# Optimization experiments

Hardware: AMD Instinct MI355X
Metric: run time of the kernel (lower is better)

Reference implementation:

```python
import jax, jax.numpy as jnp
import numpy as np

T, B, IN, H, L, C = 512, 4096, 12, 32, 10, 4


def setup_inputs() -> dict:
    key = jax.random.key(0)
    ks = jax.random.split(key, 12)
    s = 1.0 / np.sqrt(H)  # PyTorch GRU init scale ~ U(-1/sqrt(H), 1/sqrt(H))
    return {
        "x": jax.random.normal(ks[0], (T, B, IN), jnp.float32),
        "W_ih0": jax.random.normal(ks[1], (3 * H, IN), jnp.float32) * s,
        "W_hh0": jax.random.normal(ks[2], (3 * H, H), jnp.float32) * s,
        "b_ih0": jax.random.normal(ks[3], (3 * H,), jnp.float32) * s,
        "b_hh0": jax.random.normal(ks[4], (3 * H,), jnp.float32) * s,
        "W_ih": jax.random.normal(ks[5], (L - 1, 3 * H, H), jnp.float32) * s,
        "W_hh": jax.random.normal(ks[6], (L - 1, 3 * H, H), jnp.float32) * s,
        "b_ih": jax.random.normal(ks[7], (L - 1, 3 * H), jnp.float32) * s,
        "b_hh": jax.random.normal(ks[8], (L - 1, 3 * H), jnp.float32) * s,
        "fc_W": jax.random.normal(ks[9], (C, H), jnp.float32) * s,
        "fc_b": jax.random.normal(ks[10], (C,), jnp.float32) * s,
        "lengths": jax.random.randint(ks[11], (B,), 1, T + 1, jnp.int32),
    }


def gru_cell(x_t, h, Wi, Wh, bi, bh):
    # PyTorch GRU cell math
    gi = x_t @ Wi.T + bi          # [B, 3H]
    gh = h @ Wh.T + bh            # [B, 3H]
    i_r, i_z, i_n = jnp.split(gi, 3, axis=-1)
    h_r, h_z, h_n = jnp.split(gh, 3, axis=-1)
    r = jax.nn.sigmoid(i_r + h_r)
    z = jax.nn.sigmoid(i_z + h_z)
    n = jnp.tanh(i_n + r * h_n)
    return (1.0 - z) * n + z * h


def reference(x, W_ih0, W_hh0, b_ih0, b_hh0, W_ih, W_hh, b_ih, b_hh, fc_W, fc_b, lengths):
    Bn = x.shape[1]
    h0 = jnp.zeros((L, Bn, H), x.dtype)

    def step(h, x_t):
        hs = []
        inp = x_t
        for l in range(L):
            if l == 0:
                hl = gru_cell(inp, h[0], W_ih0, W_hh0, b_ih0, b_hh0)
            else:
                hl = gru_cell(inp, h[l], W_ih[l - 1], W_hh[l - 1], b_ih[l - 1], b_hh[l - 1])
            hs.append(hl)
            inp = hl
        return jnp.stack(hs), inp  # carry all-layer hidden, emit top-layer output

    _, outs = jax.lax.scan(step, h0, x)  # [T, B, H]
    idx = jnp.maximum(lengths, 1) - 1    # last valid timestep per sequence
    last = outs[idx, jnp.arange(Bn)]     # [B, H]
    logits = last @ fc_W.T + fc_b        # [B, C]
    return jax.nn.log_softmax(logits, axis=1)
```

## Files before the change

### kernel.cpp

```cpp
#include <hip/hip_runtime.h>
#include <math.h>

#define TT 512
#define BB 4096
#define IN_DIM 12
#define HH 32
#define LL 10
#define CC 4
#define NTH (LL * 64)

typedef _Float16 half8 __attribute__((ext_vector_type(8)));
typedef _Float16 half4 __attribute__((ext_vector_type(4)));
typedef float f32x4 __attribute__((ext_vector_type(4)));

#define LOG2E 1.44269504088896340736f

#define H_HI 0
#define H_LO (LL * 4 * 512)
#define X_HI (H_LO + LL * 2 * 512)
#define LDS16_TOT (X_HI + 2 * 512)

#define MFMA_(A, B, C) C = __builtin_amdgcn_mfma_f32_16x16x32_f16(A, B, C, 0, 0, 0)

__global__ __launch_bounds__(NTH, 2)
void gru_fused_mfma(const float* __restrict__ x,
                    const float* __restrict__ Wih0,
                    const float* __restrict__ Whh0,
                    const float* __restrict__ bih0,
                    const float* __restrict__ bhh0,
                    const float* __restrict__ Wih,
                    const float* __restrict__ Whh,
                    const float* __restrict__ bih,
                    const float* __restrict__ bhh,
                    const int*   __restrict__ lengths,
                    float*       __restrict__ last)
{
    __shared__ __align__(16) _Float16 lds16[LDS16_TOT];
    __shared__ int flagS[LL];
    __shared__ int rflagS[LL];

    const int tid  = threadIdx.x;
    const int w    = tid >> 6;
    const int lane = tid & 63;
    const int bi16 = lane & 15;
    const int quad = lane >> 4;
    const int bg   = blockIdx.x;

    {
        float4 z4 = make_float4(0.f, 0.f, 0.f, 0.f);
        float4* p = (float4*)lds16;
        for (int i = tid; i < LDS16_TOT / 8; i += NTH) p[i] = z4;
    }
    if (lane == 0) { flagS[w] = -1; rflagS[w] = -1; }
    __syncthreads();

    const float *Wi, *Wh, *bivec, *bhvec;
    int wistride;
    if (w == 0) { Wi = Wih0; Wh = Whh0; bivec = bih0; bhvec = bhh0; wistride = IN_DIM; }
    else {
        Wi = Wih + (size_t)(w - 1) * 96 * HH;
        Wh = Whh + (size_t)(w - 1) * 96 * HH;
        bivec = bih + (size_t)(w - 1) * 96;
        bhvec = bhh + (size_t)(w - 1) * 96;
        wistride = HH;
    }

    const int frow[12] = {0, 0, 16, 16, 32, 32, 48, 48, 64, 80, 64, 80};
    const int fchk[12] = {0, 1, 0, 1, 0, 1, 0, 1, 0, 0, 1, 1};
    half8 Whi[12], Wlo[6];
#pragma unroll
    for (int f = 0; f < 12; f++) {
        const float sc = (f < 8) ? -LOG2E : 2.0f * LOG2E;
        int row = frow[f] + bi16;
        const float* src; int kin;
        if (fchk[f] == 0) { src = Wi + (size_t)row * wistride; kin = wistride; }
        else              { src = Wh + (size_t)row * HH;       kin = HH; }
        int wloidx = (f < 8) ? (f >> 1) : (f - 6);
#pragma unroll
        for (int kk = 0; kk < 8; kk++) {
            int k = quad * 8 + kk;
            float v = (k < kin) ? src[k] * sc : 0.0f;
            _Float16 h = (_Float16)v;
            Whi[f][kk] = h;
            if (fchk[f] == 1) Wlo[wloidx][kk] = (_Float16)(v - (float)h);
        }
    }

    f32x4 biasreg[8];
#pragma unroll
    for (int ct = 0; ct < 8; ct++) {
        int g = ct >> 1, jt = ct & 1;
#pragma unroll
        for (int r = 0; r < 4; r++) {
            int j = jt * 16 + quad * 4 + r;
            float v;
            if      (g == 0) v = -(bivec[j]      + bhvec[j])      * LOG2E;
            else if (g == 1) v = -(bivec[32 + j] + bhvec[32 + j]) * LOG2E;
            else if (g == 2) v = bivec[64 + j] * (2.0f * LOG2E);
            else             v = bhvec[64 + j] * (2.0f * LOG2E);
            biasreg[ct][r] = v;
        }
    }

    int capT = -1;
    if (w == LL - 1) {
        int len = lengths[bg * 16 + bi16];
        capT = ((len < 1) ? 1 : len) - 1;
    }

    const int laneoff = lane * 8;
    const int inbase  = (w == 0) ? X_HI : (H_HI + (w - 1) * 2048);
    const int inmask  = (w == 0) ? 1 : 3;
    const int ownhi   = H_HI + w * 2048;
    const int ownlo   = H_LO + w * 1024;
    const int wibase  = (quad >> 1) * 128 + bi16 * 8 + (quad & 1) * 4;

    const int xbb = lane / 3, xkg = lane - xbb * 3;
    const int xq   = (xkg == 2) ? 1 : 0;
    const int xoff = (xkg == 1) ? 4 : 0;
    const int xidx = xq * 128 + xbb * 8 + xoff;
    const bool xlane = (w == 0) && (lane < 48);

    auto stage_x = [&](const float4& xl, int t) {
        half4 h4;
        h4[0] = (_Float16)xl.x; h4[1] = (_Float16)xl.y;
        h4[2] = (_Float16)xl.z; h4[3] = (_Float16)xl.w;
        *(half4*)(lds16 + X_HI + ((t & 1) << 9) + xidx) = h4;
    };

    if (xlane) {
        float4 x0 = *(const float4*)(x + (size_t)bg * 192 + lane * 4);
        float4 x1 = *(const float4*)(x + (size_t)BB * IN_DIM + (size_t)bg * 192 + lane * 4);
        stage_x(x0, 0);
        stage_x(x1, 1);
    }

    float hprev[8] = {0, 0, 0, 0, 0, 0, 0, 0};
    __syncthreads();

    auto substep = [&](int t) {
        half8 bxh = *(const half8*)(lds16 + inbase + ((t & inmask) << 9) + laneoff);
        half8 bhh = *(const half8*)(lds16 + ownhi + (((t + 3) & 3) << 9) + laneoff);
        half8 bhl = *(const half8*)(lds16 + ownlo + (((t + 1) & 1) << 9) + laneoff);

        f32x4 acc[8];

#pragma unroll
        for (int ct = 0; ct < 4; ct++) {
            acc[ct] = __builtin_amdgcn_mfma_f32_16x16x32_f16(
                          Whi[ct * 2 + 0], bxh, biasreg[ct], 0, 0, 0);
            MFMA_(Whi[ct * 2 + 1], bhh, acc[ct]);
            MFMA_(Whi[ct * 2 + 1], bhl, acc[ct]);
            MFMA_(Wlo[ct],         bhh, acc[ct]);
        }
#pragma unroll
        for (int jt = 0; jt < 2; jt++) {
            acc[4 + jt] = __builtin_amdgcn_mfma_f32_16x16x32_f16(
                              Whi[8 + jt], bxh, biasreg[4 + jt], 0, 0, 0);
            acc[6 + jt] = __builtin_amdgcn_mfma_f32_16x16x32_f16(
                              Whi[10 + jt], bhh, biasreg[6 + jt], 0, 0, 0);
            MFMA_(Whi[10 + jt], bhl, acc[6 + jt]);
            MFMA_(Wlo[4 + jt],  bhh, acc[6 + jt]);
        }

#pragma unroll
        for (int jt = 0; jt < 2; jt++) {
            f32x4 R = acc[0 + jt], Z = acc[2 + jt];
            f32x4 IN_ = acc[4 + jt], HN = acc[6 + jt];
            half4 h4, l4;
            float hv[4];
#pragma unroll
            for (int pr = 0; pr < 2; pr++) {
                const int r0 = pr * 2, r1 = pr * 2 + 1;
                float a0 = 1.0f + __builtin_amdgcn_exp2f(R[r0]);
                float b0 = 1.0f + __builtin_amdgcn_exp2f(Z[r0]);
                float a1 = 1.0f + __builtin_amdgcn_exp2f(R[r1]);
                float b1 = 1.0f + __builtin_amdgcn_exp2f(Z[r1]);
                float p0 = a0 * b0, p1 = a1 * b1;
                float q  = __builtin_amdgcn_rcpf(p0 * p1);
                float q0 = q * p1, q1 = q * p0;
                float rv0 = q0 * b0, zv0 = q0 * a0;
                float rv1 = q1 * b1, zv1 = q1 * a1;
                float ea0 = __builtin_amdgcn_exp2f(fmaf(rv0, HN[r0], IN_[r0]));
                float ea1 = __builtin_amdgcn_exp2f(fmaf(rv1, HN[r1], IN_[r1]));
                float d0 = ea0 + 1.0f, d1 = ea1 + 1.0f;
                float qn = __builtin_amdgcn_rcpf(d0 * d1);
                float nv0 = fmaf(-2.0f, qn * d1, 1.0f);
                float nv1 = fmaf(-2.0f, qn * d0, 1.0f);
                float h0 = fmaf(zv0, hprev[jt * 4 + r0] - nv0, nv0);
                float h1 = fmaf(zv1, hprev[jt * 4 + r1] - nv1, nv1);
                hprev[jt * 4 + r0] = h0;
                hprev[jt * 4 + r1] = h1;
                _Float16 hh0 = (_Float16)h0, hh1 = (_Float16)h1;
                h4[r0] = hh0; h4[r1] = hh1;
                l4[r0] = (_Float16)(h0 - (float)hh0);
                l4[r1] = (_Float16)(h1 - (float)hh1);
                hv[r0] = h0; hv[r1] = h1;
            }
            int wi = jt * 256 + wibase;
            *(half4*)(lds16 + ownhi + ((t & 3) << 9) + wi) = h4;
            *(half4*)(lds16 + ownlo + ((t & 1) << 9) + wi) = l4;
            if (w == LL - 1 && t == capT) {
                float4 o = make_float4(hv[0], hv[1], hv[2], hv[3]);
                *(float4*)(last + (size_t)(bg * 16 + bi16) * HH + jt * 16 + quad * 4) = o;
            }
        }
    };

    for (int t = 0; t < TT; t += 2) {
        if (w > 0) {
            while (__hip_atomic_load(&flagS[w - 1], __ATOMIC_ACQUIRE,
                                     __HIP_MEMORY_SCOPE_WORKGROUP) < t + 1)
                __builtin_amdgcn_s_sleep(1);
        }
        if (w < LL - 1) {
            while (__hip_atomic_load(&rflagS[w], __ATOMIC_ACQUIRE,
                                     __HIP_MEMORY_SCOPE_WORKGROUP) < t - 3)
                __builtin_amdgcn_s_sleep(1);
        }

        float4 xa0, xa1;
        bool dl0 = false, dl1 = false;
        if (xlane) {
            if (t + 2 < TT) {
                xa0 = *(const float4*)(x + (size_t)(t + 2) * BB * IN_DIM +
                                       (size_t)bg * 192 + lane * 4);
                dl0 = true;
            }
            if (t + 3 < TT) {
                xa1 = *(const float4*)(x + (size_t)(t + 3) * BB * IN_DIM +
                                       (size_t)bg * 192 + lane * 4);
                dl1 = true;
            }
        }

        substep(t);
        substep(t + 1);

        if (dl0) stage_x(xa0, t + 2);
        if (dl1) stage_x(xa1, t + 3);

        if (lane == 0) {
            if (w < LL - 1)
                __hip_atomic_store(&flagS[w], t + 1, __ATOMIC_RELEASE,
                                   __HIP_MEMORY_SCOPE_WORKGROUP);
            if (w > 0)
                __hip_atomic_store(&rflagS[w - 1], t + 1, __ATOMIC_RELEASE,
                                   __HIP_MEMORY_SCOPE_WORKGROUP);
        }
    }
}

__global__ __launch_bounds__(256)
void fc_head(const float* __restrict__ last,
             const float* __restrict__ fcW,
             const float* __restrict__ fcb,
             float* __restrict__ out)
{
    int b = blockIdx.x * blockDim.x + threadIdx.x;
    if (b >= BB) return;
    float lg[CC];
#pragma unroll
    for (int c = 0; c < CC; c++) lg[c] = fcb[c];
#pragma unroll
    for (int j = 0; j < HH; j++) {
        float h = last[(size_t)b * HH + j];
#pragma unroll
        for (int c = 0; c < CC; c++) lg[c] = fmaf(fcW[c * HH + j], h, lg[c]);
    }
    float m = lg[0];
#pragma unroll
    for (int c = 1; c < CC; c++) m = fmaxf(m, lg[c]);
    float s = 0.0f;
#pragma unroll
    for (int c = 0; c < CC; c++) s += __expf(lg[c] - m);
    float lse = m + logf(s);
#pragma unroll
    for (int c = 0; c < CC; c++) out[(size_t)b * CC + c] = lg[c] - lse;
}

extern "C" void kernel_launch(void* const* d_in, const int* in_sizes, int n_in,
                              void* d_out, int out_size, void* d_ws, size_t ws_size,
                              hipStream_t stream)
{
    const float* x    = (const float*)d_in[0];
    const float* Wih0 = (const float*)d_in[1];
    const float* Whh0 = (const float*)d_in[2];
    const float* bih0 = (const float*)d_in[3];
    const float* bhh0 = (const float*)d_in[4];
    const float* Wih  = (const float*)d_in[5];
    const float* Whh  = (const float*)d_in[6];
    const float* bih  = (const float*)d_in[7];
    const float* bhh  = (const float*)d_in[8];
    const float* fcW  = (const float*)d_in[9];
    const float* fcb  = (const float*)d_in[10];
    const int*   lens = (const int*)d_in[11];
    float* out = (float*)d_out;

    float* last = (float*)d_ws;

    gru_fused_mfma<<<dim3(BB / 16), dim3(NTH), 0, stream>>>(
        x, Wih0, Whh0, bih0, bhh0, Wih, Whh, bih, bhh, lens, last);

    fc_head<<<dim3(BB / 256), dim3(256), 0, stream>>>(last, fcW, fcb, out);
}
```

Before: 955.6 us.

## Pack ten GRU layers onto four waves with skewed wavefront schedule

Each workgroup now has 4 waves instead of 10, and each wave owns 2 or 3 layers. The layers run in a diagonal (skewed) schedule so that dependent cells within a round read hidden states written in earlier rounds, and inter-wave flags sync once per round. The low-half weight corrections move from registers to LDS so three layers' high-half weights fit in registers. This cuts the wave count and flag traffic and lets one wave interleave independent layer cells. The cost is more serial work per wave and extra LDS reads on every cell.

```diff
diff --git a/kernel.cpp b/kernel.cpp
--- a/kernel.cpp
+++ b/kernel.cpp
@@ -7,7 +7,7 @@
 #define HH 32
 #define LL 10
 #define CC 4
-#define NTH (LL * 64)
+#define NTH 256
 
 typedef _Float16 half8 __attribute__((ext_vector_type(8)));
 typedef _Float16 half4 __attribute__((ext_vector_type(4)));
@@ -19,10 +19,13 @@
 #define H_LO (LL * 4 * 512)
 #define X_HI (H_LO + LL * 2 * 512)
 #define LDS16_TOT (X_HI + 2 * 512)
+#define WLO_TOT (LL * 6 * 512)
 
 #define MFMA_(A, B, C) C = __builtin_amdgcn_mfma_f32_16x16x32_f16(A, B, C, 0, 0, 0)
 
-__global__ __launch_bounds__(NTH, 2)
+template<int N> struct IC { static constexpr int value = N; };
+
+__global__ __launch_bounds__(NTH, 1)
 void gru_fused_mfma(const float* __restrict__ x,
                     const float* __restrict__ Wih0,
                     const float* __restrict__ Whh0,
@@ -36,8 +39,9 @@
                     float*       __restrict__ last)
 {
     __shared__ __align__(16) _Float16 lds16[LDS16_TOT];
-    __shared__ int flagS[LL];
-    __shared__ int rflagS[LL];
+    __shared__ __align__(16) _Float16 wlo16[WLO_TOT];
+    __shared__ int flagE[3];
+    __shared__ int rflagE[3];
 
     const int tid  = threadIdx.x;
     const int w    = tid >> 6;
@@ -46,74 +50,92 @@
     const int quad = lane >> 4;
     const int bg   = blockIdx.x;
 
+    const int myStart = (w == 0) ? 0 : (w == 1) ? 2 : (w == 2) ? 5 : 8;
+    const int myCnt   = (w == 0 || w == 3) ? 2 : 3;
+
     {
         float4 z4 = make_float4(0.f, 0.f, 0.f, 0.f);
         float4* p = (float4*)lds16;
         for (int i = tid; i < LDS16_TOT / 8; i += NTH) p[i] = z4;
     }
-    if (lane == 0) { flagS[w] = -1; rflagS[w] = -1; }
-    __syncthreads();
-
-    const float *Wi, *Wh, *bivec, *bhvec;
-    int wistride;
-    if (w == 0) { Wi = Wih0; Wh = Whh0; bivec = bih0; bhvec = bhh0; wistride = IN_DIM; }
-    else {
-        Wi = Wih + (size_t)(w - 1) * 96 * HH;
-        Wh = Whh + (size_t)(w - 1) * 96 * HH;
-        bivec = bih + (size_t)(w - 1) * 96;
-        bhvec = bhh + (size_t)(w - 1) * 96;
-        wistride = HH;
-    }
+    if (tid < 3) { flagE[tid] = -1; rflagE[tid] = -1; }
 
     const int frow[12] = {0, 0, 16, 16, 32, 32, 48, 48, 64, 80, 64, 80};
     const int fchk[12] = {0, 1, 0, 1, 0, 1, 0, 1, 0, 0, 1, 1};
-    half8 Whi[12], Wlo[6];
-#pragma unroll
-    for (int f = 0; f < 12; f++) {
-        const float sc = (f < 8) ? -LOG2E : 2.0f * LOG2E;
-        int row = frow[f] + bi16;
-        const float* src; int kin;
-        if (fchk[f] == 0) { src = Wi + (size_t)row * wistride; kin = wistride; }
-        else              { src = Wh + (size_t)row * HH;       kin = HH; }
-        int wloidx = (f < 8) ? (f >> 1) : (f - 6);
-#pragma unroll
-        for (int kk = 0; kk < 8; kk++) {
-            int k = quad * 8 + kk;
-            float v = (k < kin) ? src[k] * sc : 0.0f;
-            _Float16 h = (_Float16)v;
-            Whi[f][kk] = h;
-            if (fchk[f] == 1) Wlo[wloidx][kk] = (_Float16)(v - (float)h);
-        }
-    }
-
-    f32x4 biasreg[8];
-#pragma unroll
-    for (int ct = 0; ct < 8; ct++) {
-        int g = ct >> 1, jt = ct & 1;
-#pragma unroll
-        for (int r = 0; r < 4; r++) {
-            int j = jt * 16 + quad * 4 + r;
-            float v;
-            if      (g == 0) v = -(bivec[j]      + bhvec[j])      * LOG2E;
-            else if (g == 1) v = -(bivec[32 + j] + bhvec[32 + j]) * LOG2E;
-            else if (g == 2) v = bivec[64 + j] * (2.0f * LOG2E);
-            else             v = bhvec[64 + j] * (2.0f * LOG2E);
-            biasreg[ct][r] = v;
+    const int laneoff = lane * 8;
+
+    int sigS[3], inB[3], inM[3], hiB[3], loB[3], wloB[3];
+    half8 Whi[3][12];
+    f32x4 biasreg[3][8];
+    float hprev[3][8];
+
+#pragma unroll
+    for (int s = 0; s < 3; s++) {
+        int l = myStart + s; if (l > LL - 1) l = LL - 1;
+        sigS[s] = l + (l >= 2) + (l >= 5) + (l >= 8);
+        inB[s]  = (l == 0) ? X_HI : (H_HI + (l - 1) * 2048);
+        inM[s]  = (l == 0) ? 1 : 3;
+        hiB[s]  = H_HI + l * 2048;
+        loB[s]  = H_LO + l * 1024;
+        wloB[s] = l * 3072;
+#pragma unroll
+        for (int i = 0; i < 8; i++) hprev[s][i] = 0.0f;
+
+        if (s < myCnt) {
+            const float *Wi, *Wh, *bivec, *bhvec; int wistride;
+            if (l == 0) { Wi = Wih0; Wh = Whh0; bivec = bih0; bhvec = bhh0; wistride = IN_DIM; }
+            else {
+                Wi = Wih + (size_t)(l - 1) * 96 * HH;
+                Wh = Whh + (size_t)(l - 1) * 96 * HH;
+                bivec = bih + (size_t)(l - 1) * 96;
+                bhvec = bhh + (size_t)(l - 1) * 96;
+                wistride = HH;
+            }
+#pragma unroll
+            for (int f = 0; f < 12; f++) {
+                const float sc = (f < 8) ? -LOG2E : 2.0f * LOG2E;
+                int row = frow[f] + bi16;
+                const float* src; int kin;
+                if (fchk[f] == 0) { src = Wi + (size_t)row * wistride; kin = wistride; }
+                else              { src = Wh + (size_t)row * HH;       kin = HH; }
+                half8 lo8;
+#pragma unroll
+                for (int kk = 0; kk < 8; kk++) {
+                    int k = quad * 8 + kk;
+                    float v = (k < kin) ? src[k] * sc : 0.0f;
+                    _Float16 hc = (_Float16)v;
+                    Whi[s][f][kk] = hc;
+                    lo8[kk] = (_Float16)(v - (float)hc);
+                }
+                if (fchk[f] == 1) {
+                    int wloidx = (f < 8) ? (f >> 1) : (f - 6);
+                    *(half8*)(wlo16 + wloB[s] + (wloidx << 9) + laneoff) = lo8;
+                }
+            }
+#pragma unroll
+            for (int ct = 0; ct < 8; ct++) {
+                int g = ct >> 1, jt = ct & 1;
+#pragma unroll
+                for (int rr = 0; rr < 4; rr++) {
+                    int j = jt * 16 + quad * 4 + rr;
+                    float v;
+                    if      (g == 0) v = -(bivec[j]      + bhvec[j])      * LOG2E;
+                    else if (g == 1) v = -(bivec[32 + j] + bhvec[32 + j]) * LOG2E;
+                    else if (g == 2) v = bivec[64 + j] * (2.0f * LOG2E);
+                    else             v = bhvec[64 + j] * (2.0f * LOG2E);
+                    biasreg[s][ct][rr] = v;
+                }
+            }
         }
     }
 
     int capT = -1;
-    if (w == LL - 1) {
+    if (w == 3) {
         int len = lengths[bg * 16 + bi16];
         capT = ((len < 1) ? 1 : len) - 1;
     }
 
-    const int laneoff = lane * 8;
-    const int inbase  = (w == 0) ? X_HI : (H_HI + (w - 1) * 2048);
-    const int inmask  = (w == 0) ? 1 : 3;
-    const int ownhi   = H_HI + w * 2048;
-    const int ownlo   = H_LO + w * 1024;
-    const int wibase  = (quad >> 1) * 128 + bi16 * 8 + (quad & 1) * 4;
+    const int wibase = (quad >> 1) * 128 + bi16 * 8 + (quad & 1) * 4;
 
     const int xbb = lane / 3, xkg = lane - xbb * 3;
     const int xq   = (xkg == 2) ? 1 : 0;
@@ -128,6 +150,8 @@
         *(half4*)(lds16 + X_HI + ((t & 1) << 9) + xidx) = h4;
     };
 
+    __syncthreads();
+
     if (xlane) {
         float4 x0 = *(const float4*)(x + (size_t)bg * 192 + lane * 4);
         float4 x1 = *(const float4*)(x + (size_t)BB * IN_DIM + (size_t)bg * 192 + lane * 4);
@@ -135,32 +159,34 @@
         stage_x(x1, 1);
     }
 
-    float hprev[8] = {0, 0, 0, 0, 0, 0, 0, 0};
-    __syncthreads();
-
-    auto substep = [&](int t) {
-        half8 bxh = *(const half8*)(lds16 + inbase + ((t & inmask) << 9) + laneoff);
-        half8 bhh = *(const half8*)(lds16 + ownhi + (((t + 3) & 3) << 9) + laneoff);
-        half8 bhl = *(const half8*)(lds16 + ownlo + (((t + 1) & 1) << 9) + laneoff);
+    auto cellF = [&](auto Sc, int t) {
+        constexpr int S = decltype(Sc)::value;
+        const bool lastQ = (w == 3) && (S == 1);
+        half8 bxh  = *(const half8*)(lds16 + inB[S] + ((t & inM[S]) << 9) + laneoff);
+        half8 bhh2 = *(const half8*)(lds16 + hiB[S] + (((t + 3) & 3) << 9) + laneoff);
+        half8 bhl2 = *(const half8*)(lds16 + loB[S] + (((t + 1) & 1) << 9) + laneoff);
+        half8 wl[6];
+#pragma unroll
+        for (int j = 0; j < 6; j++)
+            wl[j] = *(const half8*)(wlo16 + wloB[S] + (j << 9) + laneoff);
 
         f32x4 acc[8];
-
 #pragma unroll
         for (int ct = 0; ct < 4; ct++) {
             acc[ct] = __builtin_amdgcn_mfma_f32_16x16x32_f16(
-                          Whi[ct * 2 + 0], bxh, biasreg[ct], 0, 0, 0);
-            MFMA_(Whi[ct * 2 + 1], bhh, acc[ct]);
-            MFMA_(Whi[ct * 2 + 1], bhl, acc[ct]);
-            MFMA_(Wlo[ct],         bhh, acc[ct]);
+                          Whi[S][ct * 2 + 0], bxh, biasreg[S][ct], 0, 0, 0);
+            MFMA_(Whi[S][ct * 2 + 1], bhh2, acc[ct]);
+            MFMA_(Whi[S][ct * 2 + 1], bhl2, acc[ct]);
+            MFMA_(wl[ct],             bhh2, acc[ct]);
         }
 #pragma unroll
         for (int jt = 0; jt < 2; jt++) {
             acc[4 + jt] = __builtin_amdgcn_mfma_f32_16x16x32_f16(
-                              Whi[8 + jt], bxh, biasreg[4 + jt], 0, 0, 0);
+                              Whi[S][8 + jt], bxh, biasreg[S][4 + jt], 0, 0, 0);
             acc[6 + jt] = __builtin_amdgcn_mfma_f32_16x16x32_f16(
-                              Whi[10 + jt], bhh, biasreg[6 + jt], 0, 0, 0);
-            MFMA_(Whi[10 + jt], bhl, acc[6 + jt]);
-            MFMA_(Wlo[4 + jt],  bhh, acc[6 + jt]);
+                              Whi[S][10 + jt], bhh2, biasreg[S][6 + jt], 0, 0, 0);
+            MFMA_(Whi[S][10 + jt], bhl2, acc[6 + jt]);
+            MFMA_(wl[4 + jt],      bhh2, acc[6 + jt]);
         }
 
 #pragma unroll
@@ -187,10 +213,10 @@
                 float qn = __builtin_amdgcn_rcpf(d0 * d1);
                 float nv0 = fmaf(-2.0f, qn * d1, 1.0f);
                 float nv1 = fmaf(-2.0f, qn * d0, 1.0f);
-                float h0 = fmaf(zv0, hprev[jt * 4 + r0] - nv0, nv0);
-                float h1 = fmaf(zv1, hprev[jt * 4 + r1] - nv1, nv1);
-                hprev[jt * 4 + r0] = h0;
-                hprev[jt * 4 + r1] = h1;
+                float h0 = fmaf(zv0, hprev[S][jt * 4 + r0] - nv0, nv0);
+                float h1 = fmaf(zv1, hprev[S][jt * 4 + r1] - nv1, nv1);
+                hprev[S][jt * 4 + r0] = h0;
+                hprev[S][jt * 4 + r1] = h1;
                 _Float16 hh0 = (_Float16)h0, hh1 = (_Float16)h1;
                 h4[r0] = hh0; h4[r1] = hh1;
                 l4[r0] = (_Float16)(h0 - (float)hh0);
@@ -198,57 +224,62 @@
                 hv[r0] = h0; hv[r1] = h1;
             }
             int wi = jt * 256 + wibase;
-            *(half4*)(lds16 + ownhi + ((t & 3) << 9) + wi) = h4;
-            *(half4*)(lds16 + ownlo + ((t & 1) << 9) + wi) = l4;
-            if (w == LL - 1 && t == capT) {
+            *(half4*)(lds16 + hiB[S] + ((t & 3) << 9) + wi) = h4;
+            *(half4*)(lds16 + loB[S] + ((t & 1) << 9) + wi) = l4;
+            if (lastQ && t == capT) {
                 float4 o = make_float4(hv[0], hv[1], hv[2], hv[3]);
                 *(float4*)(last + (size_t)(bg * 16 + bi16) * HH + jt * 16 + quad * 4) = o;
             }
         }
     };
 
-    for (int t = 0; t < TT; t += 2) {
+#define RUNCELL(S, rr)                                                    \
+    do { if ((S) < myCnt) { const int t_ = (rr) - sigS[(S)];              \
+         if (t_ >= 0 && t_ < TT) cellF(IC<(S)>{}, t_); } } while (0)
+
+    for (int rnd = 0; rnd < TT + 12; rnd += 2) {
         if (w > 0) {
-            while (__hip_atomic_load(&flagS[w - 1], __ATOMIC_ACQUIRE,
-                                     __HIP_MEMORY_SCOPE_WORKGROUP) < t + 1)
+            while (__hip_atomic_load(&flagE[w - 1], __ATOMIC_ACQUIRE,
+                                     __HIP_MEMORY_SCOPE_WORKGROUP) < rnd - 1)
                 __builtin_amdgcn_s_sleep(1);
         }
-        if (w < LL - 1) {
-            while (__hip_atomic_load(&rflagS[w], __ATOMIC_ACQUIRE,
-                                     __HIP_MEMORY_SCOPE_WORKGROUP) < t - 3)
+        if (w < 3) {
+            while (__hip_atomic_load(&rflagE[w], __ATOMIC_ACQUIRE,
+                                     __HIP_MEMORY_SCOPE_WORKGROUP) < rnd - 1)
                 __builtin_amdgcn_s_sleep(1);
         }
 
         float4 xa0, xa1;
         bool dl0 = false, dl1 = false;
         if (xlane) {
-            if (t + 2 < TT) {
-                xa0 = *(const float4*)(x + (size_t)(t + 2) * BB * IN_DIM +
+            if (rnd + 2 < TT) {
+                xa0 = *(const float4*)(x + (size_t)(rnd + 2) * BB * IN_DIM +
                                        (size_t)bg * 192 + lane * 4);
                 dl0 = true;
             }
-            if (t + 3 < TT) {
-                xa1 = *(const float4*)(x + (size_t)(t + 3) * BB * IN_DIM +
+            if (rnd + 3 < TT) {
+                xa1 = *(const float4*)(x + (size_t)(rnd + 3) * BB * IN_DIM +
                                        (size_t)bg * 192 + lane * 4);
                 dl1 = true;
             }
         }
 
-        substep(t);
-        substep(t + 1);
-
-        if (dl0) stage_x(xa0, t + 2);
-        if (dl1) stage_x(xa1, t + 3);
+        RUNCELL(0, rnd);     RUNCELL(1, rnd);     RUNCELL(2, rnd);
+        RUNCELL(0, rnd + 1); RUNCELL(1, rnd + 1); RUNCELL(2, rnd + 1);
+
+        if (dl0) stage_x(xa0, rnd + 2);
+        if (dl1) stage_x(xa1, rnd + 3);
 
         if (lane == 0) {
-            if (w < LL - 1)
-                __hip_atomic_store(&flagS[w], t + 1, __ATOMIC_RELEASE,
+            if (w < 3)
+                __hip_atomic_store(&flagE[w], rnd + 1, __ATOMIC_RELEASE,
                                    __HIP_MEMORY_SCOPE_WORKGROUP);
             if (w > 0)
-                __hip_atomic_store(&rflagS[w - 1], t + 1, __ATOMIC_RELEASE,
+                __hip_atomic_store(&rflagE[w - 1], rnd + 1, __ATOMIC_RELEASE,
                                    __HIP_MEMORY_SCOPE_WORKGROUP);
         }
     }
+#undef RUNCELL
 }
 
 __global__ __launch_bounds__(256)
```

Measured after the change: 1.353 ms. +41.6%, slower.
